# Optimization experiments

Measured on AMD Instinct MI355X. Metric: run time of the kernel, lower is better.

The kernel has to match this reference:

```python
import jax, jax.numpy as jnp
import numpy as np

# Fixed genome topology (layered DAG, topologically ordered levels)
B = 4096      # batch
N_IN = 512    # input nodes
H1 = 1536     # hidden level 1
H2 = 1536     # hidden level 2
N_OUT = 512   # output nodes
FAN = 32      # fan-in per non-input node


def setup_inputs() -> dict:
    key = jax.random.key(0)
    ks = jax.random.split(key, 10)
    x = jax.random.normal(ks[0], (B, N_IN), dtype=jnp.float32)
    # level 1: sources among inputs [0, N_IN)
    src0 = jax.random.randint(ks[1], (H1 * FAN,), 0, N_IN, dtype=jnp.int32)
    dst0 = jax.random.randint(ks[2], (H1 * FAN,), 0, H1, dtype=jnp.int32)
    w0 = jax.random.normal(ks[3], (H1 * FAN,), dtype=jnp.float32) * 0.1
    # level 2: sources among inputs + level1 [0, N_IN+H1)
    src1 = jax.random.randint(ks[4], (H2 * FAN,), 0, N_IN + H1, dtype=jnp.int32)
    dst1 = jax.random.randint(ks[5], (H2 * FAN,), 0, H2, dtype=jnp.int32)
    w1 = jax.random.normal(ks[6], (H2 * FAN,), dtype=jnp.float32) * 0.1
    # output level: sources among all earlier nodes [0, N_IN+H1+H2)
    src2 = jax.random.randint(ks[7], (N_OUT * FAN,), 0, N_IN + H1 + H2, dtype=jnp.int32)
    dst2 = jax.random.randint(ks[8], (N_OUT * FAN,), 0, N_OUT, dtype=jnp.int32)
    w2 = jax.random.normal(ks[9], (N_OUT * FAN,), dtype=jnp.float32) * 0.1
    return dict(x=x, src0=src0, dst0=dst0, w0=w0,
                src1=src1, dst1=dst1, w1=w1,
                src2=src2, dst2=dst2, w2=w2)


def _level(node_values, src, dst, w, size):
    # per-edge weighted gather: [B, E]
    vals = node_values[:, src] * w
    # scatter-add into destination nodes of this level: [B, size]
    agg = jnp.zeros((node_values.shape[0], size), node_values.dtype).at[:, dst].add(vals)
    # per-node activation (genome.activation == 'relu'); relu(0)=0 matches
    # original's behavior of leaving unconnected nodes at zero
    return jax.nn.relu(agg)


def reference(x, src0, dst0, w0, src1, dst1, w1, src2, dst2, w2):
    nv = x                                        # [B, N_IN]
    h1 = _level(nv, src0, dst0, w0, H1)           # [B, H1]
    nv = jnp.concatenate([nv, h1], axis=1)        # [B, N_IN+H1]
    h2 = _level(nv, src1, dst1, w1, H2)           # [B, H2]
    nv = jnp.concatenate([nv, h2], axis=1)        # [B, N_IN+H1+H2]
    out = _level(nv, src2, dst2, w2, N_OUT)       # [B, N_OUT]
    return out
```

## Files before the change

kernel.cpp:

```cpp
#include <hip/hip_runtime.h>
#include <hip/hip_fp16.h>
#include <stdint.h>

#define BATCH 4096
#define N_IN  512
#define H1    1536
#define H2    1536
#define N_OUT 512
#define FAN   32
#define E0 (H1 * FAN)
#define E1 (H2 * FAN)
#define E2 (N_OUT * FAN)
#define ETOT (E0 + E1 + E2)
#define NNODES (H1 + H2 + N_OUT)
#define MAXDEG 128

#define OFF_EDGES 33554432
#define OFF_CNT   (OFF_EDGES + NNODES * MAXDEG * 8)

__global__ __launch_bounds__(256) void k_transpose_in(const float* __restrict__ x,
                                                      __half* __restrict__ xT) {
    __shared__ float tile[32][33];
    const int tx = threadIdx.x, ty = threadIdx.y;
    const int n0 = blockIdx.x * 32;
    const int b0 = blockIdx.y * 32;
#pragma unroll
    for (int k = 0; k < 32; k += 8)
        tile[ty + k][tx] = x[(size_t)(b0 + ty + k) * N_IN + (n0 + tx)];
    __syncthreads();
#pragma unroll
    for (int k = 0; k < 32; k += 8)
        xT[(size_t)(n0 + ty + k) * BATCH + (b0 + tx)] = __float2half_rn(tile[tx][ty + k]);
}

__global__ __launch_bounds__(256) void k_fill(const int* __restrict__ s0, const int* __restrict__ d0, const float* __restrict__ w0,
                                              const int* __restrict__ s1, const int* __restrict__ d1, const float* __restrict__ w1,
                                              const int* __restrict__ s2, const int* __restrict__ d2, const float* __restrict__ w2,
                                              int* __restrict__ cnt, int2* __restrict__ edges) {
    const int e = blockIdx.x * 256 + threadIdx.x;
    int src, node; float w;
    if (e < E0)           { src = s0[e];          node = d0[e];                w = w0[e]; }
    else if (e < E0 + E1) { int i = e - E0;       src = s1[i]; node = H1 + d1[i];        w = w1[i]; }
    else                  { int i = e - E0 - E1;  src = s2[i]; node = H1 + H2 + d2[i];   w = w2[i]; }
    const int pos = atomicAdd(&cnt[node], 1);
    if (pos < MAXDEG) edges[node * MAXDEG + pos] = make_int2(src, __float_as_int(w));
}

__global__ __launch_bounds__(256)
void k_level(const int2* __restrict__ edges,
             const int* __restrict__ cnt,
             const uint4* __restrict__ nv,
             uint4* __restrict__ outb) {
    const int lane = threadIdx.x & 63;
    const int wv   = threadIdx.x >> 6;
    const int node = (blockIdx.y << 2) | wv;
    const int col8 = (blockIdx.x << 6) | lane;

    int c = cnt[node];
    c = (c < 0) ? 0 : (c > MAXDEG ? MAXDEG : c);

    float a0 = 0.f, a1 = 0.f, a2 = 0.f, a3 = 0.f, a4 = 0.f, a5 = 0.f, a6 = 0.f, a7 = 0.f;

#define ACC8(q, W) {                                                    \
    const __half2 h0 = *(const __half2*)&(q).x;                         \
    const __half2 h1 = *(const __half2*)&(q).y;                         \
    const __half2 h2 = *(const __half2*)&(q).z;                         \
    const __half2 h3 = *(const __half2*)&(q).w;                         \
    a0 = fmaf(__low2float(h0),  (W), a0);                               \
    a1 = fmaf(__high2float(h0), (W), a1);                               \
    a2 = fmaf(__low2float(h1),  (W), a2);                               \
    a3 = fmaf(__high2float(h1), (W), a3);                               \
    a4 = fmaf(__low2float(h2),  (W), a4);                               \
    a5 = fmaf(__high2float(h2), (W), a5);                               \
    a6 = fmaf(__low2float(h3),  (W), a6);                               \
    a7 = fmaf(__high2float(h3), (W), a7); }

    for (int base = 0; base < c; base += 64) {
        const int2 my = edges[(size_t)node * MAXDEG + base + lane];
        const int m = (c - base < 64) ? (c - base) : 64;
        int j = 0;
        for (; j + 4 <= m; j += 4) {
            const int   s0i = __builtin_amdgcn_readlane(my.x, j)     & 4095;
            const int   s1i = __builtin_amdgcn_readlane(my.x, j + 1) & 4095;
            const int   s2i = __builtin_amdgcn_readlane(my.x, j + 2) & 4095;
            const int   s3i = __builtin_amdgcn_readlane(my.x, j + 3) & 4095;
            const float wa  = __int_as_float(__builtin_amdgcn_readlane(my.y, j));
            const float wb  = __int_as_float(__builtin_amdgcn_readlane(my.y, j + 1));
            const float wc  = __int_as_float(__builtin_amdgcn_readlane(my.y, j + 2));
            const float wd  = __int_as_float(__builtin_amdgcn_readlane(my.y, j + 3));
            const uint4 q0 = nv[((size_t)s0i << 9) | col8];
            const uint4 q1 = nv[((size_t)s1i << 9) | col8];
            const uint4 q2 = nv[((size_t)s2i << 9) | col8];
            const uint4 q3 = nv[((size_t)s3i << 9) | col8];
            ACC8(q0, wa);
            ACC8(q1, wb);
            ACC8(q2, wc);
            ACC8(q3, wd);
        }
        for (; j < m; ++j) {
            const int   s0i = __builtin_amdgcn_readlane(my.x, j) & 4095;
            const float wa  = __int_as_float(__builtin_amdgcn_readlane(my.y, j));
            const uint4 q0 = nv[((size_t)s0i << 9) | col8];
            ACC8(q0, wa);
        }
    }
#undef ACC8

    a0 = fmaxf(a0, 0.f); a1 = fmaxf(a1, 0.f); a2 = fmaxf(a2, 0.f); a3 = fmaxf(a3, 0.f);
    a4 = fmaxf(a4, 0.f); a5 = fmaxf(a5, 0.f); a6 = fmaxf(a6, 0.f); a7 = fmaxf(a7, 0.f);

    const __half2 h0 = __floats2half2_rn(a0, a1);
    const __half2 h1 = __floats2half2_rn(a2, a3);
    const __half2 h2 = __floats2half2_rn(a4, a5);
    const __half2 h3 = __floats2half2_rn(a6, a7);
    uint4 p;
    p.x = *(const uint32_t*)&h0; p.y = *(const uint32_t*)&h1;
    p.z = *(const uint32_t*)&h2; p.w = *(const uint32_t*)&h3;
    outb[((size_t)node << 9) | col8] = p;
}

__global__ __launch_bounds__(256) void k_transpose_out(const __half* __restrict__ outh,
                                                       float* __restrict__ out) {
    __shared__ float tile[32][33];
    const int tx = threadIdx.x, ty = threadIdx.y;
    const int n0 = blockIdx.x * 32;
    const int b0 = blockIdx.y * 32;
#pragma unroll
    for (int k = 0; k < 32; k += 8)
        tile[ty + k][tx] = __half2float(outh[(size_t)(n0 + ty + k) * BATCH + (b0 + tx)]);
    __syncthreads();
#pragma unroll
    for (int k = 0; k < 32; k += 8)
        out[(size_t)(b0 + ty + k) * N_OUT + (n0 + tx)] = tile[tx][ty + k];
}

extern "C" void kernel_launch(void* const* d_in, const int* in_sizes, int n_in,
                              void* d_out, int out_size, void* d_ws, size_t ws_size,
                              hipStream_t stream) {
    const float* x  = (const float*)d_in[0];
    const int* s0   = (const int*)d_in[1];
    const int* dd0  = (const int*)d_in[2];
    const float* w0 = (const float*)d_in[3];
    const int* s1   = (const int*)d_in[4];
    const int* dd1  = (const int*)d_in[5];
    const float* w1 = (const float*)d_in[6];
    const int* s2   = (const int*)d_in[7];
    const int* dd2  = (const int*)d_in[8];
    const float* w2 = (const float*)d_in[9];

    char* ws        = (char*)d_ws;
    uint4*    nv4   = (uint4*)ws;
    int2*     edges = (int2*)(ws + OFF_EDGES);
    int*      cnt   = (int*)(ws + OFF_CNT);

    hipMemsetAsync(cnt, 0, NNODES * sizeof(int), stream);
    k_fill<<<ETOT / 256, 256, 0, stream>>>(s0, dd0, w0, s1, dd1, w1, s2, dd2, w2, cnt, edges);

    k_transpose_in<<<dim3(N_IN / 32, BATCH / 32), dim3(32, 8), 0, stream>>>(x, (__half*)ws);

    k_level<<<dim3(8, H1 / 4), 256, 0, stream>>>(edges, cnt, nv4,
                                                 nv4 + (size_t)N_IN * 512);
    k_level<<<dim3(8, H2 / 4), 256, 0, stream>>>(edges + (size_t)H1 * MAXDEG, cnt + H1, nv4,
                                                 nv4 + (size_t)(N_IN + H1) * 512);
    k_level<<<dim3(8, N_OUT / 4), 256, 0, stream>>>(edges + (size_t)(H1 + H2) * MAXDEG, cnt + H1 + H2, nv4,
                                                    nv4 + (size_t)(N_IN + H1 + H2) * 512);

    k_transpose_out<<<dim3(N_OUT / 32, BATCH / 32), dim3(32, 8), 0, stream>>>(
        (const __half*)(ws + (size_t)(N_IN + H1 + H2) * BATCH * 2), (float*)d_out);
}
```

Measured before the change: 147.7 us.

## Pad edge lists to multiples of eight and software-pipeline gather loads

Adds a pad kernel that rounds each node's edge count up to a multiple of eight, filling the extra slots with zero-weight edges, so the level kernel no longer needs a remainder loop. The inner loop becomes a two-stage software pipeline that issues the next group of gathers before accumulating the current one, with eight loads in flight. It also sets launch bounds to request four blocks per CU. The cost is an extra tiny kernel launch, wasted work on padded edges, and higher register pressure from the doubled set of in-flight loads.

Result: slower. 152.2 us (+3.0%).

```diff
diff --git a/kernel.cpp b/kernel.cpp
--- a/kernel.cpp
+++ b/kernel.cpp
@@ -46,7 +46,18 @@
     if (pos < MAXDEG) edges[node * MAXDEG + pos] = make_int2(src, __float_as_int(w));
 }
 
-__global__ __launch_bounds__(256)
+__global__ __launch_bounds__(256) void k_pad(int* __restrict__ cnt, int2* __restrict__ edges) {
+    const int n = blockIdx.x * 256 + threadIdx.x;
+    if (n >= NNODES) return;
+    int c = cnt[n];
+    c = (c < 0) ? 0 : (c > MAXDEG ? MAXDEG : c);
+    const int cp = (c + 7) & ~7;
+    for (int p = c; p < cp; ++p)
+        edges[(size_t)n * MAXDEG + p] = make_int2(0, 0);
+    cnt[n] = cp;
+}
+
+__global__ __launch_bounds__(256, 4)
 void k_level(const int2* __restrict__ edges,
              const int* __restrict__ cnt,
              const uint4* __restrict__ nv,
@@ -56,8 +67,7 @@
     const int node = (blockIdx.y << 2) | wv;
     const int col8 = (blockIdx.x << 6) | lane;
 
-    int c = cnt[node];
-    c = (c < 0) ? 0 : (c > MAXDEG ? MAXDEG : c);
+    const int c = cnt[node];
 
     float a0 = 0.f, a1 = 0.f, a2 = 0.f, a3 = 0.f, a4 = 0.f, a5 = 0.f, a6 = 0.f, a7 = 0.f;
 
@@ -75,35 +85,52 @@
     a6 = fmaf(__low2float(h3),  (W), a6);                               \
     a7 = fmaf(__high2float(h3), (W), a7); }
 
+#define RL1(J, S, W) {                                                  \
+    S = __builtin_amdgcn_readlane(my.x, (J)) & 4095;                    \
+    W = __int_as_float(__builtin_amdgcn_readlane(my.y, (J))); }
+
+#define RLG(J, S0,S1,S2,S3, W0,W1,W2,W3)                                \
+    RL1((J),   S0, W0) RL1((J)+1, S1, W1)                               \
+    RL1((J)+2, S2, W2) RL1((J)+3, S3, W3)
+
+#define LDG(S0,S1,S2,S3, Q0,Q1,Q2,Q3)                                   \
+    Q0 = nv[((size_t)(S0) << 9) | col8];                                \
+    Q1 = nv[((size_t)(S1) << 9) | col8];                                \
+    Q2 = nv[((size_t)(S2) << 9) | col8];                                \
+    Q3 = nv[((size_t)(S3) << 9) | col8];
+
+#define ACCG(Q0,Q1,Q2,Q3, W0,W1,W2,W3)                                  \
+    ACC8(Q0, W0) ACC8(Q1, W1) ACC8(Q2, W2) ACC8(Q3, W3)
+
     for (int base = 0; base < c; base += 64) {
         const int2 my = edges[(size_t)node * MAXDEG + base + lane];
         const int m = (c - base < 64) ? (c - base) : 64;
-        int j = 0;
-        for (; j + 4 <= m; j += 4) {
-            const int   s0i = __builtin_amdgcn_readlane(my.x, j)     & 4095;
-            const int   s1i = __builtin_amdgcn_readlane(my.x, j + 1) & 4095;
-            const int   s2i = __builtin_amdgcn_readlane(my.x, j + 2) & 4095;
-            const int   s3i = __builtin_amdgcn_readlane(my.x, j + 3) & 4095;
-            const float wa  = __int_as_float(__builtin_amdgcn_readlane(my.y, j));
-            const float wb  = __int_as_float(__builtin_amdgcn_readlane(my.y, j + 1));
-            const float wc  = __int_as_float(__builtin_amdgcn_readlane(my.y, j + 2));
-            const float wd  = __int_as_float(__builtin_amdgcn_readlane(my.y, j + 3));
-            const uint4 q0 = nv[((size_t)s0i << 9) | col8];
-            const uint4 q1 = nv[((size_t)s1i << 9) | col8];
-            const uint4 q2 = nv[((size_t)s2i << 9) | col8];
-            const uint4 q3 = nv[((size_t)s3i << 9) | col8];
-            ACC8(q0, wa);
-            ACC8(q1, wb);
-            ACC8(q2, wc);
-            ACC8(q3, wd);
+
+        int sA0, sA1, sA2, sA3, sB0, sB1, sB2, sB3;
+        float wA0, wA1, wA2, wA3, wB0, wB1, wB2, wB3;
+        uint4 qA0, qA1, qA2, qA3, qB0, qB1, qB2, qB3;
+
+        RLG(0, sA0,sA1,sA2,sA3, wA0,wA1,wA2,wA3)
+        LDG(sA0,sA1,sA2,sA3, qA0,qA1,qA2,qA3)
+        RLG(4, sB0,sB1,sB2,sB3, wB0,wB1,wB2,wB3)
+        LDG(sB0,sB1,sB2,sB3, qB0,qB1,qB2,qB3)
+
+        int j = 8;
+        for (; j + 8 <= m; j += 8) {
+            ACCG(qA0,qA1,qA2,qA3, wA0,wA1,wA2,wA3)
+            RLG(j, sA0,sA1,sA2,sA3, wA0,wA1,wA2,wA3)
+            LDG(sA0,sA1,sA2,sA3, qA0,qA1,qA2,qA3)
+            ACCG(qB0,qB1,qB2,qB3, wB0,wB1,wB2,wB3)
+            RLG(j+4, sB0,sB1,sB2,sB3, wB0,wB1,wB2,wB3)
+            LDG(sB0,sB1,sB2,sB3, qB0,qB1,qB2,qB3)
         }
-        for (; j < m; ++j) {
-            const int   s0i = __builtin_amdgcn_readlane(my.x, j) & 4095;
-            const float wa  = __int_as_float(__builtin_amdgcn_readlane(my.y, j));
-            const uint4 q0 = nv[((size_t)s0i << 9) | col8];
-            ACC8(q0, wa);
-        }
+        ACCG(qA0,qA1,qA2,qA3, wA0,wA1,wA2,wA3)
+        ACCG(qB0,qB1,qB2,qB3, wB0,wB1,wB2,wB3)
     }
+#undef ACCG
+#undef LDG
+#undef RLG
+#undef RL1
 #undef ACC8
 
     a0 = fmaxf(a0, 0.f); a1 = fmaxf(a1, 0.f); a2 = fmaxf(a2, 0.f); a3 = fmaxf(a3, 0.f);
@@ -155,6 +182,7 @@
 
     hipMemsetAsync(cnt, 0, NNODES * sizeof(int), stream);
     k_fill<<<ETOT / 256, 256, 0, stream>>>(s0, dd0, w0, s1, dd1, w1, s2, dd2, w2, cnt, edges);
+    k_pad<<<(NNODES + 255) / 256, 256, 0, stream>>>(cnt, edges);
 
     k_transpose_in<<<dim3(N_IN / 32, BATCH / 32), dim3(32, 8), 0, stream>>>(x, (__half*)ws);
 
```
